# Performance work log

Measured on AMD Instinct MI355X. Metric: run time of the kernel, lower is better.

## Reference

```python
import jax, jax.numpy as jnp
import numpy as np

N_BITS = 16
V = 1 << N_BITS  # 65536 possible 16-bit patterns


def setup_inputs() -> dict:
    key = jax.random.key(0)
    k1, k2, k3 = jax.random.split(key, 3)
    B, H, T = 16, 128, 4096
    W = jax.random.normal(k1, (B, H, N_BITS), dtype=jnp.float32) * 0.5  # per-bit weights
    r = jax.random.normal(k2, (B, H), dtype=jnp.float32)                 # per-hidden phase/bias
    # x holds raw 16-bit patterns (indices into the 2^16 support)
    x = jax.random.randint(k3, (B, T), 0, V, dtype=jnp.int32)
    return {"x": x, "W": W, "r": r}


def _logits_all(W, r):
    """Logit of every one of the 2^16 representable values. [B, V]"""
    enum = jnp.arange(V, dtype=jnp.int32)
    shifts = jnp.arange(N_BITS, dtype=jnp.int32)
    bits = ((enum[:, None] >> shifts[None, :]) & 1).astype(W.dtype)  # [V, N]
    z = jnp.einsum('vn,bhn->bvh', bits, W) + r[:, None, :]           # [B, V, H]
    return jnp.cos(z).sum(axis=-1)                                    # [B, V]


def reference(x, W, r):
    """BIDE forward: log_prob(x) = logit(bits(x)) - logsumexp over all 2^N patterns."""
    logits = _logits_all(W, r)                       # [B, V]
    logZ = jax.nn.logsumexp(logits, axis=1)          # [B]  exact partition over full support
    logit_x = jnp.take_along_axis(logits, x, axis=1) # [B, T] gather by bit-pattern index
    return logit_x - logZ[:, None]
```

## Files before the change

### kernel.cpp

```cpp
#include <hip/hip_runtime.h>
#include <hip/hip_bf16.h>

#define BDIM 16
#define HDIM 128
#define TDIM 4096
#define VSZ  65536

__global__ __launch_bounds__(512) void bide_fused_logits(
    const float* __restrict__ W, const float* __restrict__ r,
    float* __restrict__ logits) {
  __shared__ float lAre[32][64];
  __shared__ float lAim[32][64];
  __shared__ float lBre[32][64];
  __shared__ float lBim[32][64];

  int bid = blockIdx.x;
  int b    = bid >> 4;
  int tile = bid & 15;
  int tlo = (tile & 3) * 64;
  int thi = (tile >> 2) * 64;
  int tid = threadIdx.x;
  int lane6 = tid & 63;
  int wrow  = tid >> 6;
  int tx = tid & 15;
  int ty = tid >> 4;

  const float* Wb = W + b * HDIM * 16;
  const float* rb = r + b * HDIM;

  float acc[2][4] = {};

  for (int kc = 0; kc < 4; ++kc) {
    int hbase = kc * 32;
#pragma unroll
    for (int i = 0; i < 4; ++i) {
      int row = wrow + i * 8;
      int h = hbase + row;
      const float* Wp = Wb + h * 16;
      int va = tlo + lane6;
      float sa = rb[h];
#pragma unroll
      for (int n = 0; n < 8; ++n)
        sa = fmaf((float)((va >> n) & 1), Wp[n], sa);
      float sina, cosa;
      __sincosf(sa, &sina, &cosa);
      lAre[row][lane6] = cosa;
      lAim[row][lane6] = sina;
      int vb = thi + lane6;
      float sb = 0.f;
#pragma unroll
      for (int n = 0; n < 8; ++n)
        sb = fmaf((float)((vb >> n) & 1), Wp[8 + n], sb);
      float sinb, cosb;
      __sincosf(sb, &sinb, &cosb);
      lBre[row][lane6] = cosb;
      lBim[row][lane6] = sinb;
    }
    __syncthreads();

#pragma unroll 4
    for (int h = 0; h < 32; ++h) {
      float4 ar = *(const float4*)&lAre[h][tx * 4];
      float4 ai = *(const float4*)&lAim[h][tx * 4];
      float2 br = *(const float2*)&lBre[h][ty * 2];
      float2 bi = *(const float2*)&lBim[h][ty * 2];
      float arr[4] = {ar.x, ar.y, ar.z, ar.w};
      float aii[4] = {ai.x, ai.y, ai.z, ai.w};
      float brr[2] = {br.x, br.y};
      float bii[2] = {bi.x, bi.y};
#pragma unroll
      for (int i2 = 0; i2 < 2; ++i2)
#pragma unroll
        for (int j = 0; j < 4; ++j) {
          acc[i2][j] = fmaf(brr[i2], arr[j], acc[i2][j]);
          acc[i2][j] = fmaf(-bii[i2], aii[j], acc[i2][j]);
        }
    }
    __syncthreads();
  }

  float* Lb = logits + b * VSZ;
#pragma unroll
  for (int i2 = 0; i2 < 2; ++i2) {
    int hi = thi + ty * 2 + i2;
    float4 v = make_float4(acc[i2][0], acc[i2][1], acc[i2][2], acc[i2][3]);
    *(float4*)&Lb[hi * 256 + tlo + tx * 4] = v;
  }
}

__global__ __launch_bounds__(1024) void bide_lse_gather(
    const float* __restrict__ logits, const int* __restrict__ x,
    float* __restrict__ out) {
  int b = blockIdx.x;
  int tid = threadIdx.x;
  int lane = tid & 63, wid = tid >> 6;
  const float4* L4 = (const float4*)(logits + b * VSZ);
  __shared__ float wred[16];
  __shared__ float s_logZ;

  float m = -1e30f;
#pragma unroll
  for (int i = 0; i < 16; ++i) {
    float4 v = L4[tid + i * 1024];
    m = fmaxf(fmaxf(fmaxf(m, v.x), v.y), fmaxf(v.z, v.w));
  }
#pragma unroll
  for (int off = 1; off < 64; off <<= 1) m = fmaxf(m, __shfl_xor(m, off, 64));
  if (lane == 0) wred[wid] = m;
  __syncthreads();
  float M = wred[0];
#pragma unroll
  for (int i = 1; i < 16; ++i) M = fmaxf(M, wred[i]);
  __syncthreads();

  float s = 0.f;
#pragma unroll
  for (int i = 0; i < 16; ++i) {
    float4 v = L4[tid + i * 1024];
    s += __expf(v.x - M) + __expf(v.y - M) + __expf(v.z - M) + __expf(v.w - M);
  }
#pragma unroll
  for (int off = 1; off < 64; off <<= 1) s += __shfl_xor(s, off, 64);
  if (lane == 0) wred[wid] = s;
  __syncthreads();
  if (tid == 0) {
    float S = 0.f;
#pragma unroll
    for (int i = 0; i < 16; ++i) S += wred[i];
    s_logZ = M + __logf(S);
  }
  __syncthreads();
  float logZ = s_logZ;

  const float* Lb = logits + b * VSZ;
  const int* xb = x + b * TDIM;
  float* ob = out + b * TDIM;
#pragma unroll
  for (int i = 0; i < 4; ++i) {
    int t = tid + i * 1024;
    ob[t] = Lb[xb[t]] - logZ;
  }
}

extern "C" void kernel_launch(void* const* d_in, const int* in_sizes, int n_in,
                              void* d_out, int out_size, void* d_ws, size_t ws_size,
                              hipStream_t stream) {
  const int*   x = (const int*)d_in[0];
  const float* W = (const float*)d_in[1];
  const float* r = (const float*)d_in[2];
  float* out = (float*)d_out;

  float* logits = (float*)d_ws;

  bide_fused_logits<<<BDIM * 16, 512, 0, stream>>>(W, r, logits);
  bide_lse_gather<<<BDIM, 1024, 0, stream>>>(logits, x, out);
}
```

Measured before the change: 83.37 us.

## Split-K the logits GEMM across block halves and parallelize logsumexp over chunks

The logits kernel now splits each 32-row h chunk between two 256-thread halves. Each thread computes a 4x4 output tile, and the two halves' partial sums are combined through shared memory before the store. The single 16-block logsumexp+gather kernel becomes two kernels: 512 blocks compute per-chunk max and sum-exp partials, and 256 blocks merge them and do the gather. This removes the low-occupancy serial reduction at the cost of an extra launch and a small partials buffer.

```diff
diff --git a/kernel.cpp b/kernel.cpp
--- a/kernel.cpp
+++ b/kernel.cpp
@@ -9,10 +9,7 @@
 __global__ __launch_bounds__(512) void bide_fused_logits(
     const float* __restrict__ W, const float* __restrict__ r,
     float* __restrict__ logits) {
-  __shared__ float lAre[32][64];
-  __shared__ float lAim[32][64];
-  __shared__ float lBre[32][64];
-  __shared__ float lBim[32][64];
+  __shared__ float smem[4 * 32 * 64];
 
   int bid = blockIdx.x;
   int b    = bid >> 4;
@@ -22,16 +19,19 @@
   int tid = threadIdx.x;
   int lane6 = tid & 63;
   int wrow  = tid >> 6;
-  int tx = tid & 15;
-  int ty = tid >> 4;
+  int half  = tid >> 8;
+  int t  = tid & 255;
+  int tx = t & 15;
+  int ty = t >> 4;
 
   const float* Wb = W + b * HDIM * 16;
   const float* rb = r + b * HDIM;
 
-  float acc[2][4] = {};
+  float acc[4][4] = {};
 
   for (int kc = 0; kc < 4; ++kc) {
     int hbase = kc * 32;
+    __syncthreads();
 #pragma unroll
     for (int i = 0; i < 4; ++i) {
       int row = wrow + i * 8;
@@ -44,8 +44,8 @@
         sa = fmaf((float)((va >> n) & 1), Wp[n], sa);
       float sina, cosa;
       __sincosf(sa, &sina, &cosa);
-      lAre[row][lane6] = cosa;
-      lAim[row][lane6] = sina;
+      smem[row * 64 + lane6]        = cosa;
+      smem[2048 + row * 64 + lane6] = sina;
       int vb = thi + lane6;
       float sb = 0.f;
 #pragma unroll
@@ -53,93 +53,117 @@
         sb = fmaf((float)((vb >> n) & 1), Wp[8 + n], sb);
       float sinb, cosb;
       __sincosf(sb, &sinb, &cosb);
-      lBre[row][lane6] = cosb;
-      lBim[row][lane6] = sinb;
+      smem[4096 + row * 64 + lane6] = cosb;
+      smem[6144 + row * 64 + lane6] = sinb;
     }
     __syncthreads();
 
+    int rbase = half * 16;
 #pragma unroll 4
-    for (int h = 0; h < 32; ++h) {
-      float4 ar = *(const float4*)&lAre[h][tx * 4];
-      float4 ai = *(const float4*)&lAim[h][tx * 4];
-      float2 br = *(const float2*)&lBre[h][ty * 2];
-      float2 bi = *(const float2*)&lBim[h][ty * 2];
+    for (int hh = 0; hh < 16; ++hh) {
+      int row = rbase + hh;
+      float4 ar = *(const float4*)&smem[row * 64 + tx * 4];
+      float4 ai = *(const float4*)&smem[2048 + row * 64 + tx * 4];
+      float4 br = *(const float4*)&smem[4096 + row * 64 + ty * 4];
+      float4 bi = *(const float4*)&smem[6144 + row * 64 + ty * 4];
       float arr[4] = {ar.x, ar.y, ar.z, ar.w};
       float aii[4] = {ai.x, ai.y, ai.z, ai.w};
-      float brr[2] = {br.x, br.y};
-      float bii[2] = {bi.x, bi.y};
+      float brr[4] = {br.x, br.y, br.z, br.w};
+      float bii[4] = {bi.x, bi.y, bi.z, bi.w};
 #pragma unroll
-      for (int i2 = 0; i2 < 2; ++i2)
+      for (int i = 0; i < 4; ++i)
 #pragma unroll
         for (int j = 0; j < 4; ++j) {
-          acc[i2][j] = fmaf(brr[i2], arr[j], acc[i2][j]);
-          acc[i2][j] = fmaf(-bii[i2], aii[j], acc[i2][j]);
+          acc[i][j] = fmaf(brr[i], arr[j], acc[i][j]);
+          acc[i][j] = fmaf(-bii[i], aii[j], acc[i][j]);
         }
     }
-    __syncthreads();
   }
 
-  float* Lb = logits + b * VSZ;
+  __syncthreads();
+  if (half) {
 #pragma unroll
-  for (int i2 = 0; i2 < 2; ++i2) {
-    int hi = thi + ty * 2 + i2;
-    float4 v = make_float4(acc[i2][0], acc[i2][1], acc[i2][2], acc[i2][3]);
-    *(float4*)&Lb[hi * 256 + tlo + tx * 4] = v;
+    for (int i = 0; i < 4; ++i)
+#pragma unroll
+      for (int j = 0; j < 4; ++j)
+        smem[(i * 4 + j) * 256 + t] = acc[i][j];
+  }
+  __syncthreads();
+  if (!half) {
+    float* Lb = logits + b * VSZ;
+#pragma unroll
+    for (int i = 0; i < 4; ++i) {
+      int hi = thi + ty * 4 + i;
+      float4 v;
+      v.x = acc[i][0] + smem[(i * 4 + 0) * 256 + t];
+      v.y = acc[i][1] + smem[(i * 4 + 1) * 256 + t];
+      v.z = acc[i][2] + smem[(i * 4 + 2) * 256 + t];
+      v.w = acc[i][3] + smem[(i * 4 + 3) * 256 + t];
+      *(float4*)&Lb[hi * 256 + tlo + tx * 4] = v;
+    }
   }
 }
 
-__global__ __launch_bounds__(1024) void bide_lse_gather(
-    const float* __restrict__ logits, const int* __restrict__ x,
-    float* __restrict__ out) {
-  int b = blockIdx.x;
+__global__ __launch_bounds__(256) void bide_lse_part(
+    const float* __restrict__ logits,
+    float* __restrict__ partM, float* __restrict__ partS) {
+  int bid = blockIdx.x;
+  int b = bid >> 5, c = bid & 31;
+  const float4* L4 = (const float4*)(logits + b * VSZ + c * 2048);
   int tid = threadIdx.x;
   int lane = tid & 63, wid = tid >> 6;
-  const float4* L4 = (const float4*)(logits + b * VSZ);
-  __shared__ float wred[16];
-  __shared__ float s_logZ;
 
-  float m = -1e30f;
-#pragma unroll
-  for (int i = 0; i < 16; ++i) {
-    float4 v = L4[tid + i * 1024];
-    m = fmaxf(fmaxf(fmaxf(m, v.x), v.y), fmaxf(v.z, v.w));
-  }
+  float4 v0 = L4[tid];
+  float4 v1 = L4[tid + 256];
+  float m = fmaxf(fmaxf(fmaxf(v0.x, v0.y), fmaxf(v0.z, v0.w)),
+                  fmaxf(fmaxf(v1.x, v1.y), fmaxf(v1.z, v1.w)));
+  __shared__ float wred[4];
+  __shared__ float wsum[4];
 #pragma unroll
   for (int off = 1; off < 64; off <<= 1) m = fmaxf(m, __shfl_xor(m, off, 64));
   if (lane == 0) wred[wid] = m;
   __syncthreads();
-  float M = wred[0];
-#pragma unroll
-  for (int i = 1; i < 16; ++i) M = fmaxf(M, wred[i]);
-  __syncthreads();
+  float M = fmaxf(fmaxf(wred[0], wred[1]), fmaxf(wred[2], wred[3]));
 
-  float s = 0.f;
-#pragma unroll
-  for (int i = 0; i < 16; ++i) {
-    float4 v = L4[tid + i * 1024];
-    s += __expf(v.x - M) + __expf(v.y - M) + __expf(v.z - M) + __expf(v.w - M);
-  }
+  float s = __expf(v0.x - M) + __expf(v0.y - M) + __expf(v0.z - M) +
+            __expf(v0.w - M) + __expf(v1.x - M) + __expf(v1.y - M) +
+            __expf(v1.z - M) + __expf(v1.w - M);
 #pragma unroll
   for (int off = 1; off < 64; off <<= 1) s += __shfl_xor(s, off, 64);
-  if (lane == 0) wred[wid] = s;
+  if (lane == 0) wsum[wid] = s;
   __syncthreads();
   if (tid == 0) {
-    float S = 0.f;
+    partM[b * 32 + c] = M;
+    partS[b * 32 + c] = wsum[0] + wsum[1] + wsum[2] + wsum[3];
+  }
+}
+
+__global__ __launch_bounds__(256) void bide_out(
+    const float* __restrict__ logits,
+    const float* __restrict__ partM, const float* __restrict__ partS,
+    const int* __restrict__ x, float* __restrict__ out) {
+  int bid = blockIdx.x;
+  int b = bid >> 4;
+  int t0 = (bid & 15) * 256;
+  int tid = threadIdx.x;
+
+  __shared__ float s_logZ;
+  if (tid < 64) {
+    float m = (tid < 32) ? partM[b * 32 + tid] : -1e30f;
+    float M = m;
 #pragma unroll
-    for (int i = 0; i < 16; ++i) S += wred[i];
-    s_logZ = M + __logf(S);
+    for (int off = 1; off < 64; off <<= 1) M = fmaxf(M, __shfl_xor(M, off, 64));
+    float s = (tid < 32) ? partS[b * 32 + tid] * __expf(m - M) : 0.f;
+#pragma unroll
+    for (int off = 1; off < 64; off <<= 1) s += __shfl_xor(s, off, 64);
+    if (tid == 0) s_logZ = M + __logf(s);
   }
   __syncthreads();
   float logZ = s_logZ;
 
-  const float* Lb = logits + b * VSZ;
-  const int* xb = x + b * TDIM;
-  float* ob = out + b * TDIM;
-#pragma unroll
-  for (int i = 0; i < 4; ++i) {
-    int t = tid + i * 1024;
-    ob[t] = Lb[xb[t]] - logZ;
-  }
+  int t = t0 + tid;
+  int vidx = x[b * TDIM + t];
+  out[b * TDIM + t] = logits[b * VSZ + vidx] - logZ;
 }
 
 extern "C" void kernel_launch(void* const* d_in, const int* in_sizes, int n_in,
@@ -151,7 +175,10 @@
   float* out = (float*)d_out;
 
   float* logits = (float*)d_ws;
+  float* partM  = logits + BDIM * VSZ;
+  float* partS  = partM + BDIM * 32;
 
   bide_fused_logits<<<BDIM * 16, 512, 0, stream>>>(W, r, logits);
-  bide_lse_gather<<<BDIM, 1024, 0, stream>>>(logits, x, out);
+  bide_lse_part<<<BDIM * 32, 256, 0, stream>>>(logits, partM, partS);
+  bide_out<<<BDIM * TDIM / 256, 256, 0, stream>>>(logits, partM, partS, x, out);
 }
```

Result: faster. 78.47 us (-5.9%).

## Use bf16 MFMA for logits and fuse partial logsumexp into logits kernel

Applied to the files above, without the earlier changes.

Replaces the scalar FMA complex-product accumulation with bf16 MFMA 16x16x32, packing cos and negated sin as a K-pair so one matrix multiply gives the real part. Each logits block also computes a per-tile max and sum-exp, so the second kernel no longer re-reads all logits. The gather kernel becomes a wide launch of 256 blocks that merges 16 partials per batch. This trades fp32 precision for bf16 inputs, which may raise error, and uses an XOR-swizzled shared staging buffer.

```diff
diff --git a/kernel.cpp b/kernel.cpp
--- a/kernel.cpp
+++ b/kernel.cpp
@@ -6,13 +6,20 @@
 #define TDIM 4096
 #define VSZ  65536
 
-__global__ __launch_bounds__(512) void bide_fused_logits(
+typedef __attribute__((ext_vector_type(8))) short bf16x8;
+typedef __attribute__((ext_vector_type(4))) float f32x4;
+
+static __device__ __forceinline__ unsigned int f2bf(float f) {
+  unsigned int u = __float_as_uint(f);
+  return (u + 0x7fffu + ((u >> 16) & 1u)) >> 16;
+}
+
+__global__ __launch_bounds__(512) void bide_logits_mfma(
     const float* __restrict__ W, const float* __restrict__ r,
-    float* __restrict__ logits) {
-  __shared__ float lAre[32][64];
-  __shared__ float lAim[32][64];
-  __shared__ float lBre[32][64];
-  __shared__ float lBim[32][64];
+    float* __restrict__ logits, float* __restrict__ partM,
+    float* __restrict__ partS) {
+  __shared__ unsigned int stg[2][64 * 32];
+  __shared__ float red[16];
 
   int bid = blockIdx.x;
   int b    = bid >> 4;
@@ -20,126 +27,119 @@
   int tlo = (tile & 3) * 64;
   int thi = (tile >> 2) * 64;
   int tid = threadIdx.x;
-  int lane6 = tid & 63;
-  int wrow  = tid >> 6;
-  int tx = tid & 15;
-  int ty = tid >> 4;
+
+  int tab  = tid >> 8;
+  int srow = tid & 63;
+  int grp  = (tid >> 6) & 3;
+  int sval = (tab ? tlo : thi) + srow;
+  int woff = tab ? 0 : 8;
+
+  int l = tid & 63;
+  int w = tid >> 6;
+  int rowblk = w & 3, colhalf = w >> 2;
+  int r15 = l & 15, kl = l >> 4;
+  int arow  = rowblk * 16 + r15;
+  int brow0 = colhalf * 32 + r15;
+  int brow1 = brow0 + 16;
 
   const float* Wb = W + b * HDIM * 16;
   const float* rb = r + b * HDIM;
 
-  float acc[2][4] = {};
+  f32x4 acc0 = {0.f, 0.f, 0.f, 0.f};
+  f32x4 acc1 = {0.f, 0.f, 0.f, 0.f};
+
+  const bf16x8* U8 = (const bf16x8*)stg[0];
+  const bf16x8* V8 = (const bf16x8*)stg[1];
+  unsigned int* stow = stg[tab];
 
   for (int kc = 0; kc < 4; ++kc) {
     int hbase = kc * 32;
+    __syncthreads();
 #pragma unroll
-    for (int i = 0; i < 4; ++i) {
-      int row = wrow + i * 8;
-      int h = hbase + row;
-      const float* Wp = Wb + h * 16;
-      int va = tlo + lane6;
-      float sa = rb[h];
+    for (int e = 0; e < 8; ++e) {
+      int hp = grp * 8 + e;
+      int h = hbase + hp;
+      const float* Wp = Wb + h * 16 + woff;
+      float sacc = tab ? rb[h] : 0.f;
 #pragma unroll
       for (int n = 0; n < 8; ++n)
-        sa = fmaf((float)((va >> n) & 1), Wp[n], sa);
-      float sina, cosa;
-      __sincosf(sa, &sina, &cosa);
-      lAre[row][lane6] = cosa;
-      lAim[row][lane6] = sina;
-      int vb = thi + lane6;
-      float sb = 0.f;
-#pragma unroll
-      for (int n = 0; n < 8; ++n)
-        sb = fmaf((float)((vb >> n) & 1), Wp[8 + n], sb);
-      float sinb, cosb;
-      __sincosf(sb, &sinb, &cosb);
-      lBre[row][lane6] = cosb;
-      lBim[row][lane6] = sinb;
+        sacc = fmaf((float)((sval >> n) & 1), Wp[n], sacc);
+      float sn, cs;
+      __sincosf(sacc, &sn, &cs);
+      if (!tab) sn = -sn;
+      stow[srow * 32 + (hp ^ ((srow & 7) << 2))] = f2bf(cs) | (f2bf(sn) << 16);
     }
     __syncthreads();
 
-#pragma unroll 4
-    for (int h = 0; h < 32; ++h) {
-      float4 ar = *(const float4*)&lAre[h][tx * 4];
-      float4 ai = *(const float4*)&lAim[h][tx * 4];
-      float2 br = *(const float2*)&lBre[h][ty * 2];
-      float2 bi = *(const float2*)&lBim[h][ty * 2];
-      float arr[4] = {ar.x, ar.y, ar.z, ar.w};
-      float aii[4] = {ai.x, ai.y, ai.z, ai.w};
-      float brr[2] = {br.x, br.y};
-      float bii[2] = {bi.x, bi.y};
 #pragma unroll
-      for (int i2 = 0; i2 < 2; ++i2)
-#pragma unroll
-        for (int j = 0; j < 4; ++j) {
-          acc[i2][j] = fmaf(brr[i2], arr[j], acc[i2][j]);
-          acc[i2][j] = fmaf(-bii[i2], aii[j], acc[i2][j]);
-        }
+    for (int ks = 0; ks < 2; ++ks) {
+      bf16x8 a  = U8[arow  * 8 + ((ks * 4 + kl) ^ (arow  & 7))];
+      bf16x8 b0 = V8[brow0 * 8 + ((ks * 4 + kl) ^ (brow0 & 7))];
+      bf16x8 b1 = V8[brow1 * 8 + ((ks * 4 + kl) ^ (brow1 & 7))];
+      acc0 = __builtin_amdgcn_mfma_f32_16x16x32_bf16(a, b0, acc0, 0, 0, 0);
+      acc1 = __builtin_amdgcn_mfma_f32_16x16x32_bf16(a, b1, acc1, 0, 0, 0);
     }
-    __syncthreads();
   }
 
   float* Lb = logits + b * VSZ;
+  int orow = thi + rowblk * 16 + 4 * kl;
+  int ocol = tlo + colhalf * 32 + r15;
 #pragma unroll
-  for (int i2 = 0; i2 < 2; ++i2) {
-    int hi = thi + ty * 2 + i2;
-    float4 v = make_float4(acc[i2][0], acc[i2][1], acc[i2][2], acc[i2][3]);
-    *(float4*)&Lb[hi * 256 + tlo + tx * 4] = v;
+  for (int q = 0; q < 4; ++q) {
+    Lb[(orow + q) * 256 + ocol]      = acc0[q];
+    Lb[(orow + q) * 256 + ocol + 16] = acc1[q];
   }
-}
 
-__global__ __launch_bounds__(1024) void bide_lse_gather(
-    const float* __restrict__ logits, const int* __restrict__ x,
-    float* __restrict__ out) {
-  int b = blockIdx.x;
-  int tid = threadIdx.x;
-  int lane = tid & 63, wid = tid >> 6;
-  const float4* L4 = (const float4*)(logits + b * VSZ);
-  __shared__ float wred[16];
-  __shared__ float s_logZ;
-
-  float m = -1e30f;
-#pragma unroll
-  for (int i = 0; i < 16; ++i) {
-    float4 v = L4[tid + i * 1024];
-    m = fmaxf(fmaxf(fmaxf(m, v.x), v.y), fmaxf(v.z, v.w));
-  }
+  float m = fmaxf(fmaxf(fmaxf(acc0[0], acc0[1]), fmaxf(acc0[2], acc0[3])),
+                  fmaxf(fmaxf(acc1[0], acc1[1]), fmaxf(acc1[2], acc1[3])));
 #pragma unroll
   for (int off = 1; off < 64; off <<= 1) m = fmaxf(m, __shfl_xor(m, off, 64));
-  if (lane == 0) wred[wid] = m;
+  if (l == 0) red[w] = m;
   __syncthreads();
-  float M = wred[0];
+  float M = red[0];
 #pragma unroll
-  for (int i = 1; i < 16; ++i) M = fmaxf(M, wred[i]);
-  __syncthreads();
-
+  for (int i = 1; i < 8; ++i) M = fmaxf(M, red[i]);
   float s = 0.f;
 #pragma unroll
-  for (int i = 0; i < 16; ++i) {
-    float4 v = L4[tid + i * 1024];
-    s += __expf(v.x - M) + __expf(v.y - M) + __expf(v.z - M) + __expf(v.w - M);
-  }
+  for (int q = 0; q < 4; ++q)
+    s += __expf(acc0[q] - M) + __expf(acc1[q] - M);
 #pragma unroll
   for (int off = 1; off < 64; off <<= 1) s += __shfl_xor(s, off, 64);
-  if (lane == 0) wred[wid] = s;
+  if (l == 0) red[8 + w] = s;
   __syncthreads();
   if (tid == 0) {
     float S = 0.f;
 #pragma unroll
-    for (int i = 0; i < 16; ++i) S += wred[i];
-    s_logZ = M + __logf(S);
+    for (int i = 0; i < 8; ++i) S += red[8 + i];
+    partM[bid] = M;
+    partS[bid] = S;
+  }
+}
+
+__global__ __launch_bounds__(256) void bide_out(
+    const float* __restrict__ logits,
+    const float* __restrict__ partM, const float* __restrict__ partS,
+    const int* __restrict__ x, float* __restrict__ out) {
+  int bid = blockIdx.x;
+  int b   = bid >> 4;
+  int seg = bid & 15;
+  int tid = threadIdx.x;
+  __shared__ float s_logZ;
+  if (tid < 64) {
+    float m  = (tid < 16) ? partM[b * 16 + tid] : -1e30f;
+    float sv = (tid < 16) ? partS[b * 16 + tid] : 0.f;
+    float M = m;
+#pragma unroll
+    for (int off = 1; off < 16; off <<= 1) M = fmaxf(M, __shfl_xor(M, off, 16));
+    float z = sv * __expf(m - M);
+#pragma unroll
+    for (int off = 1; off < 16; off <<= 1) z += __shfl_xor(z, off, 16);
+    if (tid == 0) s_logZ = M + __logf(z);
   }
   __syncthreads();
-  float logZ = s_logZ;
-
-  const float* Lb = logits + b * VSZ;
-  const int* xb = x + b * TDIM;
-  float* ob = out + b * TDIM;
-#pragma unroll
-  for (int i = 0; i < 4; ++i) {
-    int t = tid + i * 1024;
-    ob[t] = Lb[xb[t]] - logZ;
-  }
+  int t = seg * 256 + tid;
+  int vidx = x[b * TDIM + t];
+  out[b * TDIM + t] = logits[b * VSZ + vidx] - s_logZ;
 }
 
 extern "C" void kernel_launch(void* const* d_in, const int* in_sizes, int n_in,
@@ -151,7 +151,9 @@
   float* out = (float*)d_out;
 
   float* logits = (float*)d_ws;
+  float* partM  = logits + BDIM * VSZ;
+  float* partS  = partM + 256;
 
-  bide_fused_logits<<<BDIM * 16, 512, 0, stream>>>(W, r, logits);
-  bide_lse_gather<<<BDIM, 1024, 0, stream>>>(logits, x, out);
+  bide_logits_mfma<<<BDIM * 16, 512, 0, stream>>>(W, r, logits, partM, partS);
+  bide_out<<<BDIM * TDIM / 256, 256, 0, stream>>>(logits, partM, partS, x, out);
 }
```

Measured after the change: 70.85 us. 15.0% less time.
